# Kernel optimization log

Hardware: AMD Instinct MI355X
Metric: run time of the kernel (lower is better)

The kernel has to match this reference:

```python
import jax, jax.numpy as jnp
import numpy as np
import math

L = 4      # model_layers
D = 512    # model_filters
H = 32     # heads = max(D//16, 1)
DH = D // H  # 16
S = 1024   # dataset_dimension == max_len == seq_len
B = 2
EPS = 1e-5


def setup_inputs() -> dict:
    key = jax.random.key(0)
    ks = jax.random.split(key, 12)
    scale = 0.02
    n = lambda k, shape: jax.random.normal(k, shape, dtype=jnp.float32) * scale
    return {
        "x": jax.random.normal(ks[0], (B, S), dtype=jnp.float32),
        "Winit": n(ks[1], (D,)),               # init_linear weight (1->D)
        "binit": jnp.zeros((D,), jnp.float32),
        "Wq": n(ks[2], (L, D, D)), "bq": jnp.zeros((L, D), jnp.float32),
        "Wk": n(ks[3], (L, D, D)), "bk": jnp.zeros((L, D), jnp.float32),
        "Wv": n(ks[4], (L, D, D)), "bv": jnp.zeros((L, D), jnp.float32),
        "Er": jax.random.normal(ks[5], (L, S, DH), dtype=jnp.float32) * scale,
        "Wlin": n(ks[6], (L, D, D)), "blin": jnp.zeros((L, D), jnp.float32),
        "ln_g": jnp.ones((L, D), jnp.float32), "ln_b": jnp.zeros((L, D), jnp.float32),
        "Wout": n(ks[7], (D, 1)),              # output_linear, no bias
    }


def layernorm(x, g, b):
    mu = jnp.mean(x, axis=-1, keepdims=True)
    var = jnp.mean(jnp.square(x - mu), axis=-1, keepdims=True)
    return (x - mu) * jax.lax.rsqrt(var + EPS) * g + b


def rel_attn(h, Wq, bq, Wk, bk, Wv, bv, Er):
    # h: [B, S, D]
    b_, s_, _ = h.shape
    q = (h @ Wq + bq).reshape(b_, s_, H, DH).transpose(0, 2, 1, 3)  # [B,H,S,dh]
    k = (h @ Wk + bk).reshape(b_, s_, H, DH).transpose(0, 2, 1, 3)
    v = (h @ Wv + bv).reshape(b_, s_, H, DH).transpose(0, 2, 1, 3)
    # relative-position term with skew trick (seq_len == max_len -> full Er)
    QEr = jnp.einsum('bhsd,td->bhst', q, Er)                  # [B,H,S,S]
    padded = jnp.pad(QEr, ((0, 0), (0, 0), (0, 0), (1, 0)))   # pad left of last dim
    Srel = padded.reshape(b_, H, s_ + 1, s_)[:, :, 1:, :]     # skew
    scores = (jnp.einsum('bhsd,bhtd->bhst', q, k) + Srel) / math.sqrt(DH)
    mask = jnp.tril(jnp.ones((s_, s_), dtype=bool))           # causal
    scores = jnp.where(mask, scores, -jnp.inf)
    p = jax.nn.softmax(scores, axis=-1)
    o = jnp.einsum('bhst,bhtd->bhsd', p, v)
    return o.transpose(0, 2, 1, 3).reshape(b_, s_, D)


def reference(x, Winit, binit, Wq, bq, Wk, bk, Wv, bv, Er, Wlin, blin, ln_g, ln_b, Wout):
    # init_linear(1->D) on scalar per position, then exact gelu
    h = jax.nn.gelu(x[..., None] * Winit + binit, approximate=False)  # [B,S,D]
    for l in range(L):
        a = rel_attn(h, Wq[l], bq[l], Wk[l], bk[l], Wv[l], bv[l], Er[l])
        y = layernorm(a @ Wlin[l] + blin[l], ln_g[l], ln_b[l])
        h = h + jax.nn.gelu(y, approximate=False)
    return h.sum(axis=-2) @ Wout  # [B,1]
```

## Files before the change

### kernel.cpp

```cpp
#include <hip/hip_runtime.h>
#include <math.h>

#define NL 4
#define DIM 512
#define NH 32
#define DHD 16
#define SEQ 1024
#define NB 2
#define LN_EPS 1e-5f
#define NEGF (-1e30f)
#define QSC 0.36067376022224085f

typedef _Float16 half4 __attribute__((ext_vector_type(4)));
typedef _Float16 half8 __attribute__((ext_vector_type(8)));
typedef float floatx4 __attribute__((ext_vector_type(4)));

__device__ __forceinline__ float gelu_exact(float x) {
    return 0.5f * x * (1.0f + erff(x * 0.70710678118654752f));
}

__device__ __forceinline__ void async16(const void* g, void* l) {
    __builtin_amdgcn_global_load_lds(
        (const __attribute__((address_space(1))) void*)g,
        (__attribute__((address_space(3))) void*)l, 16, 0, 0);
}

__global__ __launch_bounds__(256) void k_prep_all(const float* __restrict__ Wq,
        const float* __restrict__ Wk, const float* __restrict__ Wv,
        const float* __restrict__ Wlin, const float* __restrict__ bq,
        const float* __restrict__ bk, const float* __restrict__ bv,
        const float* __restrict__ Er, const float* __restrict__ x,
        const float* __restrict__ Wi, const float* __restrict__ bi,
        _Float16* __restrict__ Wqkvt, _Float16* __restrict__ Wlint,
        float* __restrict__ bqkv, _Float16* __restrict__ Erh,
        float* __restrict__ h, _Float16* __restrict__ hf) {
    __shared__ _Float16 lt[64][72];
    const int u = blockIdx.x;
    const int tid = threadIdx.x;
    if (u < 1024) {
        const int kx = u & 7, ny = (u >> 3) & 7, mz = u >> 6;
        const int l = mz >> 2, which = mz & 3;
        const float* src = (which == 0) ? Wq : (which == 1) ? Wk : (which == 2) ? Wv : Wlin;
        src += (size_t)l * 262144;
        const float scale = (which == 0) ? QSC : 1.0f;
        _Float16* dst = (which < 3) ? (Wqkvt + (size_t)l * 786432 + (size_t)which * 262144)
                                    : (Wlint + (size_t)l * 262144);
        const int k0 = kx << 6, n0 = ny << 6;
        #pragma unroll
        for (int p = 0; p < 4; p++) {
            int kl = (p << 4) + (tid >> 4);
            int n4 = (tid & 15) << 2;
            float4 wv = *(const float4*)(src + (size_t)(k0 + kl) * 512 + n0 + n4);
            lt[n4 + 0][kl] = (_Float16)(wv.x * scale);
            lt[n4 + 1][kl] = (_Float16)(wv.y * scale);
            lt[n4 + 2][kl] = (_Float16)(wv.z * scale);
            lt[n4 + 3][kl] = (_Float16)(wv.w * scale);
        }
        __syncthreads();
        int nl = tid >> 2, k16 = (tid & 3) << 4;
        float4* d4 = (float4*)(dst + (size_t)(n0 + nl) * 512 + k0 + k16);
        const float4* s4 = (const float4*)&lt[nl][k16];
        d4[0] = s4[0];
        d4[1] = s4[1];
    } else if (u < 2048) {
        int idx0 = ((u - 1024) << 10) + (tid << 2);
        int d = idx0 & 511, bs = idx0 >> 9;
        float xs = x[bs];
        float4 wv = *(const float4*)(Wi + d);
        float4 bv = *(const float4*)(bi + d);
        float4 r;
        r.x = gelu_exact(xs * wv.x + bv.x);
        r.y = gelu_exact(xs * wv.y + bv.y);
        r.z = gelu_exact(xs * wv.z + bv.z);
        r.w = gelu_exact(xs * wv.w + bv.w);
        *(float4*)(h + idx0) = r;
        half4 rh = {(_Float16)r.x, (_Float16)r.y, (_Float16)r.z, (_Float16)r.w};
        *(half4*)(hf + idx0) = rh;
    } else {
        int idx = ((u - 2048) << 8) + tid;
        if (idx < NL * 1536) {
            int l = idx / 1536, j = idx % 1536;
            int which = j >> 9, jj = j & 511;
            float val = (which == 0) ? bq[l * 512 + jj] * QSC
                      : (which == 1) ? bk[l * 512 + jj] : bv[l * 512 + jj];
            bqkv[idx] = val;
        }
        int e = idx - NL * 1536;
        if (e >= 0 && e < NL * SEQ * DHD) Erh[e] = (_Float16)Er[e];
    }
}

__global__ __launch_bounds__(256) void k_gemm_qkv(const _Float16* __restrict__ A,
        const _Float16* __restrict__ Bt, const float* __restrict__ bias,
        _Float16* __restrict__ o16) {
    __shared__ _Float16 As[64 * 32];
    __shared__ _Float16 Bs[128 * 32];
    const int tid = threadIdx.x;
    const int w = tid >> 6, lane = tid & 63;
    const int nn = lane & 15, qd = lane >> 4;
    const int wm = (w & 1) << 5, wn = (w >> 1) << 6;
    const int m0 = blockIdx.x << 6, n0 = blockIdx.y << 7;
    const int ar = (w << 4) + (lane >> 2);
    const int ac = (lane & 3) << 3;
    const _Float16* Ag  = A  + (size_t)(m0 + ar) * 512 + ac;
    const _Float16* Bg0 = Bt + (size_t)(n0 + (w << 5) + (lane >> 2)) * 512 + ac;
    const _Float16* Bg1 = Bg0 + 16 * 512;
    _Float16* Al  = As + ((w << 4) << 5);
    _Float16* Bl0 = Bs + ((w << 5) << 5);
    _Float16* Bl1 = Bl0 + (16 << 5);
    floatx4 acc[2][4] = {};
    for (int k0 = 0; k0 < 512; k0 += 32) {
        __syncthreads();
        async16(Ag + k0, Al);
        async16(Bg0 + k0, Bl0);
        async16(Bg1 + k0, Bl1);
        __syncthreads();
        half8 af[2], bf[4];
        #pragma unroll
        for (int t = 0; t < 2; t++)
            af[t] = *(const half8*)&As[((wm + (t << 4) + nn) << 5) + (qd << 3)];
        #pragma unroll
        for (int t = 0; t < 4; t++)
            bf[t] = *(const half8*)&Bs[((wn + (t << 4) + nn) << 5) + (qd << 3)];
        #pragma unroll
        for (int ti = 0; ti < 2; ti++)
            #pragma unroll
            for (int tj = 0; tj < 4; tj++)
                acc[ti][tj] = __builtin_amdgcn_mfma_f32_16x16x32_f16(
                        af[ti], bf[tj], acc[ti][tj], 0, 0, 0);
    }
    float bv4[4];
    #pragma unroll
    for (int tj = 0; tj < 4; tj++) bv4[tj] = bias[n0 + wn + (tj << 4) + nn];
    #pragma unroll
    for (int ti = 0; ti < 2; ti++) {
        int rowg = m0 + wm + (ti << 4) + (qd << 2);
        #pragma unroll
        for (int tj = 0; tj < 4; tj++) {
            int colg = n0 + wn + (tj << 4) + nn;
            int which = colg >> 9, ci = colg & 511;
            _Float16* op = o16 + (size_t)which * 1048576 + (size_t)rowg * 512 + ci;
            #pragma unroll
            for (int r = 0; r < 4; r++)
                op[(size_t)r * 512] = (_Float16)(acc[ti][tj][r] + bv4[tj]);
        }
    }
}

__global__ __launch_bounds__(256, 4) void k_attn_mfma(const _Float16* __restrict__ q,
        const _Float16* __restrict__ k, const _Float16* __restrict__ v,
        const _Float16* __restrict__ Er, float* __restrict__ Osp,
        float* __restrict__ ml) {
    __shared__ _Float16 Ks[256][20];
    __shared__ _Float16 Vts[16][264];
    __shared__ float Rel[4][16][84];
    const int tid = threadIdx.x;
    const int wid = tid >> 6, lane = tid & 63;
    const int nn = lane & 15, a4 = (lane >> 4) << 2;
    const int b_ = blockIdx.x >> 5, h_ = blockIdx.x & 31;
    const int qt = blockIdx.y, sp = blockIdx.z;
    const int nch = qt + 1;
    const int hsp = (nch + 1) >> 1;
    const int c_lo = sp ? hsp : 0, c_hi = sp ? nch : hsp;
    const int r0 = qt << 6;
    const int s0w = r0 + (wid << 4);
    const int t_ = tid >> 2, c4 = (tid & 3) << 2;

    half4 qf = *(const half4*)(q + ((size_t)(b_ * SEQ + s0w + nn)) * DIM + h_ * DHD + a4);
    floatx4 O = {0.f, 0.f, 0.f, 0.f};
    float m = NEGF, lsum = 0.f;

    for (int cg = c_lo; cg < c_hi; cg += 4) {
        const int cge = (cg + 4 < c_hi) ? (cg + 4) : c_hi;
        __syncthreads();
        for (int g = 0; g < cge - cg; g++) {
            int rl = (g << 6) + t_;
            size_t gb = ((size_t)(b_ * SEQ + (cg << 6) + rl)) * DIM + h_ * DHD + c4;
            *(half4*)&Ks[rl][c4] = *(const half4*)(k + gb);
            half4 vv4 = *(const half4*)(v + gb);
            Vts[c4 + 0][rl] = vv4.x;
            Vts[c4 + 1][rl] = vv4.y;
            Vts[c4 + 2][rl] = vv4.z;
            Vts[c4 + 3][rl] = vv4.w;
        }
        __syncthreads();
        for (int c = cg; c < cge; c++) {
            const int ct = c << 6;
            const int ctl = (c - cg) << 6;
            const int jbw = 1008 - s0w + ct;
            #pragma unroll
            for (int jt = 0; jt < 5; jt++) {
                int j = jbw + (jt << 4) + nn;
                j = (j < SEQ - 1) ? j : (SEQ - 1);
                half4 ef = *(const half4*)(Er + (size_t)j * DHD + a4);
                floatx4 racc = {0.f, 0.f, 0.f, 0.f};
                racc = __builtin_amdgcn_mfma_f32_16x16x16f16(ef, qf, racc, 0, 0, 0);
                *(floatx4*)&Rel[wid][nn][(jt << 4) + a4] = racc;
            }
            float st[4][4];
            const bool diag = (ct == r0);
            #pragma unroll
            for (int tt = 0; tt < 4; tt++) {
                half4 kf = *(const half4*)&Ks[ctl + (tt << 4) + nn][a4];
                floatx4 sacc = {0.f, 0.f, 0.f, 0.f};
                sacc = __builtin_amdgcn_mfma_f32_16x16x16f16(kf, qf, sacc, 0, 0, 0);
                #pragma unroll
                for (int r = 0; r < 4; r++) {
                    int tl = (tt << 4) + a4 + r;
                    float sv = sacc[r] + Rel[wid][nn][15 - nn + tl];
                    if (diag && (tl > (wid << 4) + nn)) sv = NEGF;
                    st[tt][r] = sv;
                }
            }
            float cmax = NEGF;
            #pragma unroll
            for (int tt = 0; tt < 4; tt++)
                #pragma unroll
                for (int r = 0; r < 4; r++) cmax = fmaxf(cmax, st[tt][r]);
            cmax = fmaxf(cmax, __shfl_xor(cmax, 16));
            cmax = fmaxf(cmax, __shfl_xor(cmax, 32));
            float mnew = fmaxf(m, cmax);
            float alpha = exp2f(m - mnew);
            m = mnew;
            float csum = 0.f;
            half4 pf[4];
            #pragma unroll
            for (int tt = 0; tt < 4; tt++) {
                float p0e = exp2f(st[tt][0] - mnew);
                float p1e = exp2f(st[tt][1] - mnew);
                float p2e = exp2f(st[tt][2] - mnew);
                float p3e = exp2f(st[tt][3] - mnew);
                csum += (p0e + p1e) + (p2e + p3e);
                half4 ph4 = {(_Float16)p0e, (_Float16)p1e, (_Float16)p2e, (_Float16)p3e};
                pf[tt] = ph4;
            }
            csum += __shfl_xor(csum, 16);
            csum += __shfl_xor(csum, 32);
            lsum = lsum * alpha + csum;
            O[0] *= alpha; O[1] *= alpha; O[2] *= alpha; O[3] *= alpha;
            #pragma unroll
            for (int tt = 0; tt < 4; tt++) {
                half4 vf = *(const half4*)&Vts[nn][ctl + (tt << 4) + a4];
                O = __builtin_amdgcn_mfma_f32_16x16x16f16(vf, pf[tt], O, 0, 0, 0);
            }
        }
    }
    float* op = Osp + (size_t)sp * 1048576
              + ((size_t)(b_ * SEQ + s0w + nn)) * DIM + h_ * DHD + a4;
    *(float4*)op = make_float4(O[0], O[1], O[2], O[3]);
    if (a4 == 0) {
        float2* mlp = (float2*)ml;
        mlp[((size_t)((sp * NB + b_) * NH + h_)) * SEQ + s0w + nn] = make_float2(m, lsum);
    }
}

__global__ __launch_bounds__(256) void k_gemm_lin(const float* __restrict__ Osp,
        const float* __restrict__ ml, const _Float16* __restrict__ Bt,
        const float* __restrict__ bias, float* __restrict__ y) {
    __shared__ _Float16 As[64][40];
    __shared__ _Float16 Bs[64 * 32];
    const int tid = threadIdx.x;
    const int w = tid >> 6, lane = tid & 63;
    const int nn = lane & 15, qd = lane >> 4;
    const int wm = (w & 1) << 5, wn = (w >> 1) << 5;
    const int m0 = blockIdx.x << 6, n0 = blockIdx.y << 6;
    const int sr = tid >> 2, sc8 = (tid & 3) << 3;
    const int rowg = m0 + sr;
    const int bb = rowg >> 10, ss = rowg & 1023;
    const float2* mlp = (const float2*)ml;
    const _Float16* Bg = Bt + (size_t)(n0 + (w << 4) + (lane >> 2)) * 512 + ((lane & 3) << 3);
    _Float16* Bl = Bs + ((w << 4) << 5);
    floatx4 acc[2][2] = {};
    for (int k0 = 0; k0 < 512; k0 += 32) {
        __syncthreads();
        async16(Bg + k0, Bl);
        {
            int col = k0 + sc8;
            int hh = col >> 4;
            float2 ml0 = mlp[((size_t)((0 * NB + bb) * NH + hh)) * SEQ + ss];
            float2 ml1 = mlp[((size_t)((1 * NB + bb) * NH + hh)) * SEQ + ss];
            float msx = fmaxf(ml0.x, ml1.x);
            float w0 = exp2f(ml0.x - msx), w1 = exp2f(ml1.x - msx);
            float inv = 1.0f / (ml0.y * w0 + ml1.y * w1);
            w0 *= inv; w1 *= inv;
            const float* p0 = Osp + (size_t)rowg * 512 + col;
            const float* p1 = p0 + 1048576;
            float4 a0 = *(const float4*)(p0);
            float4 a1 = *(const float4*)(p0 + 4);
            float4 b0 = *(const float4*)(p1);
            float4 b1 = *(const float4*)(p1 + 4);
            half8 av = { (_Float16)(a0.x * w0 + b0.x * w1), (_Float16)(a0.y * w0 + b0.y * w1),
                         (_Float16)(a0.z * w0 + b0.z * w1), (_Float16)(a0.w * w0 + b0.w * w1),
                         (_Float16)(a1.x * w0 + b1.x * w1), (_Float16)(a1.y * w0 + b1.y * w1),
                         (_Float16)(a1.z * w0 + b1.z * w1), (_Float16)(a1.w * w0 + b1.w * w1) };
            *(half8*)&As[sr][sc8] = av;
        }
        __syncthreads();
        half8 af[2], bf[2];
        #pragma unroll
        for (int t = 0; t < 2; t++) {
            af[t] = *(const half8*)&As[wm + (t << 4) + nn][qd << 3];
            bf[t] = *(const half8*)&Bs[((wn + (t << 4) + nn) << 5) + (qd << 3)];
        }
        #pragma unroll
        for (int ti = 0; ti < 2; ti++)
            #pragma unroll
            for (int tj = 0; tj < 2; tj++)
                acc[ti][tj] = __builtin_amdgcn_mfma_f32_16x16x32_f16(
                        af[ti], bf[tj], acc[ti][tj], 0, 0, 0);
    }
    float bv2[2];
    #pragma unroll
    for (int tj = 0; tj < 2; tj++) bv2[tj] = bias[n0 + wn + (tj << 4) + nn];
    #pragma unroll
    for (int ti = 0; ti < 2; ti++) {
        int rg = m0 + wm + (ti << 4) + (qd << 2);
        #pragma unroll
        for (int tj = 0; tj < 2; tj++) {
            int colg = n0 + wn + (tj << 4) + nn;
            float* op = y + (size_t)rg * 512 + colg;
            #pragma unroll
            for (int r = 0; r < 4; r++)
                op[(size_t)r * 512] = acc[ti][tj][r] + bv2[tj];
        }
    }
}

__global__ __launch_bounds__(256) void k_ln_gelu_res(const float* __restrict__ y,
        const float* __restrict__ gam, const float* __restrict__ bet,
        float* __restrict__ h, _Float16* __restrict__ hf) {
    __shared__ float red[8];
    int row = blockIdx.x, tid = threadIdx.x;
    const float* yr = y + (size_t)row * DIM;
    float v0 = yr[tid], v1 = yr[tid + 256];
    float sum = v0 + v1, sq = v0 * v0 + v1 * v1;
    #pragma unroll
    for (int off = 32; off > 0; off >>= 1) {
        sum += __shfl_down(sum, off);
        sq  += __shfl_down(sq, off);
    }
    if ((tid & 63) == 0) { red[tid >> 6] = sum; red[4 + (tid >> 6)] = sq; }
    __syncthreads();
    float ts = red[0] + red[1] + red[2] + red[3];
    float tq = red[4] + red[5] + red[6] + red[7];
    float mu = ts * (1.0f / DIM);
    float var = tq * (1.0f / DIM) - mu * mu;
    float rs = rsqrtf(var + LN_EPS);
    float z0 = (v0 - mu) * rs * gam[tid] + bet[tid];
    float z1 = (v1 - mu) * rs * gam[tid + 256] + bet[tid + 256];
    size_t base = (size_t)row * DIM;
    float nh0 = h[base + tid] + gelu_exact(z0);
    float nh1 = h[base + tid + 256] + gelu_exact(z1);
    h[base + tid] = nh0;
    h[base + tid + 256] = nh1;
    hf[base + tid] = (_Float16)nh0;
    hf[base + tid + 256] = (_Float16)nh1;
}

__global__ __launch_bounds__(256) void k_colsum(const float* __restrict__ h,
        float* __restrict__ partial) {
    int bt = blockIdx.x;
    int b_ = bt >> 4, t = bt & 15;
    int tid = threadIdx.x;
    #pragma unroll
    for (int half = 0; half < 2; half++) {
        int d = half * 256 + tid;
        float acc = 0.f;
        for (int i = 0; i < 64; i++)
            acc += h[((size_t)(b_ * SEQ + t * 64 + i)) * DIM + d];
        partial[(size_t)bt * DIM + d] = acc;
    }
}

__global__ __launch_bounds__(256) void k_final(const float* __restrict__ partial,
        const float* __restrict__ Wout, float* __restrict__ out) {
    __shared__ float red[4][2];
    int tid = threadIdx.x;
    float acc0 = 0.f, acc1 = 0.f;
    #pragma unroll
    for (int half = 0; half < 2; half++) {
        int d = half * 256 + tid;
        float w = Wout[d];
        float s0 = 0.f, s1 = 0.f;
        for (int t = 0; t < 16; t++) {
            s0 += partial[t * DIM + d];
            s1 += partial[(16 + t) * DIM + d];
        }
        acc0 += s0 * w;
        acc1 += s1 * w;
    }
    #pragma unroll
    for (int off = 32; off > 0; off >>= 1) {
        acc0 += __shfl_down(acc0, off);
        acc1 += __shfl_down(acc1, off);
    }
    if ((tid & 63) == 0) { red[tid >> 6][0] = acc0; red[tid >> 6][1] = acc1; }
    __syncthreads();
    if (tid == 0) {
        out[0] = red[0][0] + red[1][0] + red[2][0] + red[3][0];
        out[1] = red[0][1] + red[1][1] + red[2][1] + red[3][1];
    }
}

extern "C" void kernel_launch(void* const* d_in, const int* in_sizes, int n_in,
                              void* d_out, int out_size, void* d_ws, size_t ws_size,
                              hipStream_t stream) {
    const float* x    = (const float*)d_in[0];
    const float* Wi   = (const float*)d_in[1];
    const float* bi   = (const float*)d_in[2];
    const float* Wq   = (const float*)d_in[3];
    const float* bq   = (const float*)d_in[4];
    const float* Wk   = (const float*)d_in[5];
    const float* bk   = (const float*)d_in[6];
    const float* Wv   = (const float*)d_in[7];
    const float* bv   = (const float*)d_in[8];
    const float* Er   = (const float*)d_in[9];
    const float* Wlin = (const float*)d_in[10];
    const float* blin = (const float*)d_in[11];
    const float* lng  = (const float*)d_in[12];
    const float* lnb  = (const float*)d_in[13];
    const float* Wout = (const float*)d_in[14];
    float* out = (float*)d_out;

    float* ws = (float*)d_ws;
    const size_t N1 = 1048576;
    float*     h     = ws;
    _Float16*  hf    = (_Float16*)(ws + N1);
    _Float16*  qh    = (_Float16*)(ws + N1 + N1/2);
    float*     y     = ws + 3 * N1;
    _Float16*  Wqkvt = (_Float16*)(ws + 4 * N1 + N1/2);
    _Float16*  Wlint = (_Float16*)(ws + 6 * N1);
    float*     bqkv  = ws + 6 * N1 + N1/2;
    _Float16*  Erh   = (_Float16*)(ws + 6 * N1 + N1/2 + 8192);
    float*     Osp   = ws + 7 * N1;
    float*     ml    = ws + 9 * N1;
    float*     pa    = ws + 9 * N1 + 262144 + 64;

    k_prep_all<<<dim3(2328), dim3(256), 0, stream>>>(Wq, Wk, Wv, Wlin, bq, bk, bv,
            Er, x, Wi, bi, Wqkvt, Wlint, bqkv, Erh, h, hf);
    for (int l = 0; l < NL; l++) {
        k_gemm_qkv<<<dim3(32, 12), dim3(256), 0, stream>>>(
                hf, Wqkvt + (size_t)l * 786432, bqkv + l * 1536, qh);
        k_attn_mfma<<<dim3(NB * NH, 16, 2), dim3(256), 0, stream>>>(
                qh, qh + 1048576, qh + 2097152, Erh + (size_t)l * 16384, Osp, ml);
        k_gemm_lin<<<dim3(32, 8), dim3(256), 0, stream>>>(
                Osp, ml, Wlint + (size_t)l * 262144, blin + l * 512, y);
        k_ln_gelu_res<<<dim3(NB * SEQ), dim3(256), 0, stream>>>(
                y, lng + l * 512, lnb + l * 512, h, hf);
    }
    k_colsum<<<dim3(32), dim3(256), 0, stream>>>(h, pa);
    k_final<<<dim3(1), dim3(256), 0, stream>>>(pa, Wout, out);
}
```

Baseline: 336.8 us.

## Pair causal query tiles in attention, emit fp16 output, widen GEMM k-steps, warp-per-row LN

Attention no longer splits the key range into two halves merged later. Each block now processes a balanced pair of query tiles (y and 15-y) and writes normalized fp16 output directly, so the fp32 partial outputs and max/sum buffers go away. The linear GEMM therefore becomes a plain fp16 async-load GEMM. The QKV and linear GEMMs load 64-wide k-slices per barrier pair, halving synchronizations. LayerNorm uses one wavefront per row with vectorized float4 loads and no shared-memory reduction. The cost is half as many attention blocks, which means less parallelism, plus larger shared-memory tiles in the GEMMs.

```diff
diff --git a/kernel.cpp b/kernel.cpp
--- a/kernel.cpp
+++ b/kernel.cpp
@@ -93,41 +93,44 @@
 __global__ __launch_bounds__(256) void k_gemm_qkv(const _Float16* __restrict__ A,
         const _Float16* __restrict__ Bt, const float* __restrict__ bias,
         _Float16* __restrict__ o16) {
-    __shared__ _Float16 As[64 * 32];
-    __shared__ _Float16 Bs[128 * 32];
+    __shared__ _Float16 As[2 * 64 * 32];
+    __shared__ _Float16 Bs[2 * 128 * 32];
     const int tid = threadIdx.x;
     const int w = tid >> 6, lane = tid & 63;
     const int nn = lane & 15, qd = lane >> 4;
     const int wm = (w & 1) << 5, wn = (w >> 1) << 6;
     const int m0 = blockIdx.x << 6, n0 = blockIdx.y << 7;
-    const int ar = (w << 4) + (lane >> 2);
-    const int ac = (lane & 3) << 3;
-    const _Float16* Ag  = A  + (size_t)(m0 + ar) * 512 + ac;
-    const _Float16* Bg0 = Bt + (size_t)(n0 + (w << 5) + (lane >> 2)) * 512 + ac;
-    const _Float16* Bg1 = Bg0 + 16 * 512;
-    _Float16* Al  = As + ((w << 4) << 5);
-    _Float16* Bl0 = Bs + ((w << 5) << 5);
-    _Float16* Bl1 = Bl0 + (16 << 5);
+    const int l2r = lane >> 2, l2c = (lane & 3) << 3;
+    const _Float16* Ag = A + (size_t)(m0 + (w << 4) + l2r) * 512 + l2c;
+    const _Float16* Bg = Bt + (size_t)(n0 + (w << 5) + l2r) * 512 + l2c;
+    _Float16* Al = As + (w << 9);
+    _Float16* Bl = Bs + (w << 10);
     floatx4 acc[2][4] = {};
-    for (int k0 = 0; k0 < 512; k0 += 32) {
-        __syncthreads();
-        async16(Ag + k0, Al);
-        async16(Bg0 + k0, Bl0);
-        async16(Bg1 + k0, Bl1);
-        __syncthreads();
-        half8 af[2], bf[4];
-        #pragma unroll
-        for (int t = 0; t < 2; t++)
-            af[t] = *(const half8*)&As[((wm + (t << 4) + nn) << 5) + (qd << 3)];
-        #pragma unroll
-        for (int t = 0; t < 4; t++)
-            bf[t] = *(const half8*)&Bs[((wn + (t << 4) + nn) << 5) + (qd << 3)];
-        #pragma unroll
-        for (int ti = 0; ti < 2; ti++)
-            #pragma unroll
-            for (int tj = 0; tj < 4; tj++)
-                acc[ti][tj] = __builtin_amdgcn_mfma_f32_16x16x32_f16(
-                        af[ti], bf[tj], acc[ti][tj], 0, 0, 0);
+    for (int k0 = 0; k0 < 512; k0 += 64) {
+        __syncthreads();
+        #pragma unroll
+        for (int p = 0; p < 2; p++) {
+            async16(Ag + k0 + (p << 5), Al + (p << 11));
+            async16(Bg + k0 + (p << 5), Bl + (p << 12));
+            async16(Bg + k0 + (p << 5) + (16 << 9), Bl + (p << 12) + (16 << 5));
+        }
+        __syncthreads();
+        #pragma unroll
+        for (int ks = 0; ks < 2; ks++) {
+            half8 af[2], bf[4];
+            #pragma unroll
+            for (int t = 0; t < 2; t++)
+                af[t] = *(const half8*)&As[(ks << 11) + ((wm + (t << 4) + nn) << 5) + (qd << 3)];
+            #pragma unroll
+            for (int t = 0; t < 4; t++)
+                bf[t] = *(const half8*)&Bs[(ks << 12) + ((wn + (t << 4) + nn) << 5) + (qd << 3)];
+            #pragma unroll
+            for (int ti = 0; ti < 2; ti++)
+                #pragma unroll
+                for (int tj = 0; tj < 4; tj++)
+                    acc[ti][tj] = __builtin_amdgcn_mfma_f32_16x16x32_f16(
+                            af[ti], bf[tj], acc[ti][tj], 0, 0, 0);
+        }
     }
     float bv4[4];
     #pragma unroll
@@ -147,35 +150,99 @@
     }
 }
 
+__global__ __launch_bounds__(256) void k_gemm_lin(const _Float16* __restrict__ A,
+        const _Float16* __restrict__ Bt, const float* __restrict__ bias,
+        float* __restrict__ y) {
+    __shared__ _Float16 As[2 * 64 * 32];
+    __shared__ _Float16 Bs[2 * 64 * 32];
+    const int tid = threadIdx.x;
+    const int w = tid >> 6, lane = tid & 63;
+    const int nn = lane & 15, qd = lane >> 4;
+    const int wm = (w & 1) << 5, wn = (w >> 1) << 5;
+    const int m0 = blockIdx.x << 6, n0 = blockIdx.y << 6;
+    const int l2r = lane >> 2, l2c = (lane & 3) << 3;
+    const _Float16* Ag = A + (size_t)(m0 + (w << 4) + l2r) * 512 + l2c;
+    const _Float16* Bg = Bt + (size_t)(n0 + (w << 4) + l2r) * 512 + l2c;
+    _Float16* Al = As + (w << 9);
+    _Float16* Bl = Bs + (w << 9);
+    floatx4 acc[2][2] = {};
+    for (int k0 = 0; k0 < 512; k0 += 64) {
+        __syncthreads();
+        #pragma unroll
+        for (int p = 0; p < 2; p++) {
+            async16(Ag + k0 + (p << 5), Al + (p << 11));
+            async16(Bg + k0 + (p << 5), Bl + (p << 11));
+        }
+        __syncthreads();
+        #pragma unroll
+        for (int ks = 0; ks < 2; ks++) {
+            half8 af[2], bf[2];
+            #pragma unroll
+            for (int t = 0; t < 2; t++) {
+                af[t] = *(const half8*)&As[(ks << 11) + ((wm + (t << 4) + nn) << 5) + (qd << 3)];
+                bf[t] = *(const half8*)&Bs[(ks << 11) + ((wn + (t << 4) + nn) << 5) + (qd << 3)];
+            }
+            #pragma unroll
+            for (int ti = 0; ti < 2; ti++)
+                #pragma unroll
+                for (int tj = 0; tj < 2; tj++)
+                    acc[ti][tj] = __builtin_amdgcn_mfma_f32_16x16x32_f16(
+                            af[ti], bf[tj], acc[ti][tj], 0, 0, 0);
+        }
+    }
+    float bv2[2];
+    #pragma unroll
+    for (int tj = 0; tj < 2; tj++) bv2[tj] = bias[n0 + wn + (tj << 4) + nn];
+    #pragma unroll
+    for (int ti = 0; ti < 2; ti++) {
+        int rg = m0 + wm + (ti << 4) + (qd << 2);
+        #pragma unroll
+        for (int tj = 0; tj < 2; tj++) {
+            int colg = n0 + wn + (tj << 4) + nn;
+            float* op = y + (size_t)rg * 512 + colg;
+            #pragma unroll
+            for (int r = 0; r < 4; r++)
+                op[(size_t)r * 512] = acc[ti][tj][r] + bv2[tj];
+        }
+    }
+}
+
 __global__ __launch_bounds__(256, 4) void k_attn_mfma(const _Float16* __restrict__ q,
         const _Float16* __restrict__ k, const _Float16* __restrict__ v,
-        const _Float16* __restrict__ Er, float* __restrict__ Osp,
-        float* __restrict__ ml) {
+        const _Float16* __restrict__ Er, _Float16* __restrict__ aout) {
     __shared__ _Float16 Ks[256][20];
-    __shared__ _Float16 Vts[16][264];
-    __shared__ float Rel[4][16][84];
+    __shared__ _Float16 Vts[16][268];
+    __shared__ float Rel[4][16][80];
     const int tid = threadIdx.x;
     const int wid = tid >> 6, lane = tid & 63;
     const int nn = lane & 15, a4 = (lane >> 4) << 2;
     const int b_ = blockIdx.x >> 5, h_ = blockIdx.x & 31;
-    const int qt = blockIdx.y, sp = blockIdx.z;
-    const int nch = qt + 1;
-    const int hsp = (nch + 1) >> 1;
-    const int c_lo = sp ? hsp : 0, c_hi = sp ? nch : hsp;
-    const int r0 = qt << 6;
-    const int s0w = r0 + (wid << 4);
+    const int y = blockIdx.y;
     const int t_ = tid >> 2, c4 = (tid & 3) << 2;
-
-    half4 qf = *(const half4*)(q + ((size_t)(b_ * SEQ + s0w + nn)) * DIM + h_ * DHD + a4);
-    floatx4 O = {0.f, 0.f, 0.f, 0.f};
-    float m = NEGF, lsum = 0.f;
-
-    for (int cg = c_lo; cg < c_hi; cg += 4) {
-        const int cge = (cg + 4 < c_hi) ? (cg + 4) : c_hi;
-        __syncthreads();
-        for (int g = 0; g < cge - cg; g++) {
+    const int r0p[2] = {64 * y, 64 * (15 - y)};
+    const int R = r0p[1] + 64;
+
+    half4 qf[2];
+    floatx4 O[2];
+    float m[2], lsum[2];
+    #pragma unroll
+    for (int ph = 0; ph < 2; ph++) {
+        int s0w = r0p[ph] + (wid << 4);
+        qf[ph] = *(const half4*)(q + ((size_t)(b_ * SEQ + s0w + nn)) * DIM + h_ * DHD + a4);
+        O[ph] = (floatx4){0.f, 0.f, 0.f, 0.f};
+        m[ph] = NEGF;
+        lsum[ph] = 0.f;
+    }
+
+    for (int part = 0; part < 4; part++) {
+        const int p0 = part << 8;
+        if (p0 >= R) break;
+        const int pend = (R < p0 + 256) ? R : (p0 + 256);
+        __syncthreads();
+        const int ng = (pend - p0) >> 6;
+        for (int g = 0; g < ng; g++) {
             int rl = (g << 6) + t_;
-            size_t gb = ((size_t)(b_ * SEQ + (cg << 6) + rl)) * DIM + h_ * DHD + c4;
+            size_t gb = ((size_t)(b_ * SEQ + p0 + rl)) * DIM + h_ * DHD + c4;
             *(half4*)&Ks[rl][c4] = *(const half4*)(k + gb);
             half4 vv4 = *(const half4*)(v + gb);
             Vts[c4 + 0][rl] = vv4.x;
@@ -184,177 +251,123 @@
             Vts[c4 + 3][rl] = vv4.w;
         }
         __syncthreads();
-        for (int c = cg; c < cge; c++) {
-            const int ct = c << 6;
-            const int ctl = (c - cg) << 6;
-            const int jbw = 1008 - s0w + ct;
-            #pragma unroll
-            for (int jt = 0; jt < 5; jt++) {
-                int j = jbw + (jt << 4) + nn;
-                j = (j < SEQ - 1) ? j : (SEQ - 1);
-                half4 ef = *(const half4*)(Er + (size_t)j * DHD + a4);
-                floatx4 racc = {0.f, 0.f, 0.f, 0.f};
-                racc = __builtin_amdgcn_mfma_f32_16x16x16f16(ef, qf, racc, 0, 0, 0);
-                *(floatx4*)&Rel[wid][nn][(jt << 4) + a4] = racc;
-            }
-            float st[4][4];
-            const bool diag = (ct == r0);
-            #pragma unroll
-            for (int tt = 0; tt < 4; tt++) {
-                half4 kf = *(const half4*)&Ks[ctl + (tt << 4) + nn][a4];
-                floatx4 sacc = {0.f, 0.f, 0.f, 0.f};
-                sacc = __builtin_amdgcn_mfma_f32_16x16x16f16(kf, qf, sacc, 0, 0, 0);
-                #pragma unroll
-                for (int r = 0; r < 4; r++) {
-                    int tl = (tt << 4) + a4 + r;
-                    float sv = sacc[r] + Rel[wid][nn][15 - nn + tl];
-                    if (diag && (tl > (wid << 4) + nn)) sv = NEGF;
-                    st[tt][r] = sv;
+        #pragma unroll
+        for (int ph = 0; ph < 2; ph++) {
+            const int r0 = r0p[ph];
+            const int s0w = r0 + (wid << 4);
+            const int hi = (r0 + 64 < pend) ? (r0 + 64) : pend;
+            for (int ct = p0; ct < hi; ct += 64) {
+                const int ctl = ct - p0;
+                const int jbw = 1008 - s0w + ct;
+                #pragma unroll
+                for (int jt = 0; jt < 5; jt++) {
+                    int j = jbw + (jt << 4) + nn;
+                    j = (j < SEQ - 1) ? j : (SEQ - 1);
+                    half4 ef = *(const half4*)(Er + (size_t)j * DHD + a4);
+                    floatx4 racc = {0.f, 0.f, 0.f, 0.f};
+                    racc = __builtin_amdgcn_mfma_f32_16x16x16f16(ef, qf[ph], racc, 0, 0, 0);
+                    *(floatx4*)&Rel[wid][nn][(jt << 4) + a4] = racc;
+                }
+                float st[4][4];
+                const bool diag = (ct == r0);
+                #pragma unroll
+                for (int tt = 0; tt < 4; tt++) {
+                    half4 kf = *(const half4*)&Ks[ctl + (tt << 4) + nn][a4];
+                    floatx4 sacc = {0.f, 0.f, 0.f, 0.f};
+                    sacc = __builtin_amdgcn_mfma_f32_16x16x16f16(kf, qf[ph], sacc, 0, 0, 0);
+                    #pragma unroll
+                    for (int r = 0; r < 4; r++) {
+                        int tl = (tt << 4) + a4 + r;
+                        float sv = sacc[r] + Rel[wid][nn][15 - nn + tl];
+                        if (diag && (tl > (wid << 4) + nn)) sv = NEGF;
+                        st[tt][r] = sv;
+                    }
+                }
+                float cmax = NEGF;
+                #pragma unroll
+                for (int tt = 0; tt < 4; tt++)
+                    #pragma unroll
+                    for (int r = 0; r < 4; r++) cmax = fmaxf(cmax, st[tt][r]);
+                cmax = fmaxf(cmax, __shfl_xor(cmax, 16));
+                cmax = fmaxf(cmax, __shfl_xor(cmax, 32));
+                float mnew = fmaxf(m[ph], cmax);
+                float alpha = exp2f(m[ph] - mnew);
+                m[ph] = mnew;
+                float csum = 0.f;
+                half4 pf[4];
+                #pragma unroll
+                for (int tt = 0; tt < 4; tt++) {
+                    float p0e = exp2f(st[tt][0] - mnew);
+                    float p1e = exp2f(st[tt][1] - mnew);
+                    float p2e = exp2f(st[tt][2] - mnew);
+                    float p3e = exp2f(st[tt][3] - mnew);
+                    csum += (p0e + p1e) + (p2e + p3e);
+                    half4 ph4 = {(_Float16)p0e, (_Float16)p1e, (_Float16)p2e, (_Float16)p3e};
+                    pf[tt] = ph4;
+                }
+                lsum[ph] = lsum[ph] * alpha + csum;
+                O[ph][0] *= alpha; O[ph][1] *= alpha; O[ph][2] *= alpha; O[ph][3] *= alpha;
+                #pragma unroll
+                for (int tt = 0; tt < 4; tt++) {
+                    half4 vf = *(const half4*)&Vts[nn][ctl + (tt << 4) + a4];
+                    O[ph] = __builtin_amdgcn_mfma_f32_16x16x16f16(vf, pf[tt], O[ph], 0, 0, 0);
                 }
             }
-            float cmax = NEGF;
-            #pragma unroll
-            for (int tt = 0; tt < 4; tt++)
-                #pragma unroll
-                for (int r = 0; r < 4; r++) cmax = fmaxf(cmax, st[tt][r]);
-            cmax = fmaxf(cmax, __shfl_xor(cmax, 16));
-            cmax = fmaxf(cmax, __shfl_xor(cmax, 32));
-            float mnew = fmaxf(m, cmax);
-            float alpha = exp2f(m - mnew);
-            m = mnew;
-            float csum = 0.f;
-            half4 pf[4];
-            #pragma unroll
-            for (int tt = 0; tt < 4; tt++) {
-                float p0e = exp2f(st[tt][0] - mnew);
-                float p1e = exp2f(st[tt][1] - mnew);
-                float p2e = exp2f(st[tt][2] - mnew);
-                float p3e = exp2f(st[tt][3] - mnew);
-                csum += (p0e + p1e) + (p2e + p3e);
-                half4 ph4 = {(_Float16)p0e, (_Float16)p1e, (_Float16)p2e, (_Float16)p3e};
-                pf[tt] = ph4;
-            }
-            csum += __shfl_xor(csum, 16);
-            csum += __shfl_xor(csum, 32);
-            lsum = lsum * alpha + csum;
-            O[0] *= alpha; O[1] *= alpha; O[2] *= alpha; O[3] *= alpha;
-            #pragma unroll
-            for (int tt = 0; tt < 4; tt++) {
-                half4 vf = *(const half4*)&Vts[nn][ctl + (tt << 4) + a4];
-                O = __builtin_amdgcn_mfma_f32_16x16x16f16(vf, pf[tt], O, 0, 0, 0);
-            }
-        }
-    }
-    float* op = Osp + (size_t)sp * 1048576
-              + ((size_t)(b_ * SEQ + s0w + nn)) * DIM + h_ * DHD + a4;
-    *(float4*)op = make_float4(O[0], O[1], O[2], O[3]);
-    if (a4 == 0) {
-        float2* mlp = (float2*)ml;
-        mlp[((size_t)((sp * NB + b_) * NH + h_)) * SEQ + s0w + nn] = make_float2(m, lsum);
-    }
-}
-
-__global__ __launch_bounds__(256) void k_gemm_lin(const float* __restrict__ Osp,
-        const float* __restrict__ ml, const _Float16* __restrict__ Bt,
-        const float* __restrict__ bias, float* __restrict__ y) {
-    __shared__ _Float16 As[64][40];
-    __shared__ _Float16 Bs[64 * 32];
-    const int tid = threadIdx.x;
-    const int w = tid >> 6, lane = tid & 63;
-    const int nn = lane & 15, qd = lane >> 4;
-    const int wm = (w & 1) << 5, wn = (w >> 1) << 5;
-    const int m0 = blockIdx.x << 6, n0 = blockIdx.y << 6;
-    const int sr = tid >> 2, sc8 = (tid & 3) << 3;
-    const int rowg = m0 + sr;
-    const int bb = rowg >> 10, ss = rowg & 1023;
-    const float2* mlp = (const float2*)ml;
-    const _Float16* Bg = Bt + (size_t)(n0 + (w << 4) + (lane >> 2)) * 512 + ((lane & 3) << 3);
-    _Float16* Bl = Bs + ((w << 4) << 5);
-    floatx4 acc[2][2] = {};
-    for (int k0 = 0; k0 < 512; k0 += 32) {
-        __syncthreads();
-        async16(Bg + k0, Bl);
-        {
-            int col = k0 + sc8;
-            int hh = col >> 4;
-            float2 ml0 = mlp[((size_t)((0 * NB + bb) * NH + hh)) * SEQ + ss];
-            float2 ml1 = mlp[((size_t)((1 * NB + bb) * NH + hh)) * SEQ + ss];
-            float msx = fmaxf(ml0.x, ml1.x);
-            float w0 = exp2f(ml0.x - msx), w1 = exp2f(ml1.x - msx);
-            float inv = 1.0f / (ml0.y * w0 + ml1.y * w1);
-            w0 *= inv; w1 *= inv;
-            const float* p0 = Osp + (size_t)rowg * 512 + col;
-            const float* p1 = p0 + 1048576;
-            float4 a0 = *(const float4*)(p0);
-            float4 a1 = *(const float4*)(p0 + 4);
-            float4 b0 = *(const float4*)(p1);
-            float4 b1 = *(const float4*)(p1 + 4);
-            half8 av = { (_Float16)(a0.x * w0 + b0.x * w1), (_Float16)(a0.y * w0 + b0.y * w1),
-                         (_Float16)(a0.z * w0 + b0.z * w1), (_Float16)(a0.w * w0 + b0.w * w1),
-                         (_Float16)(a1.x * w0 + b1.x * w1), (_Float16)(a1.y * w0 + b1.y * w1),
-                         (_Float16)(a1.z * w0 + b1.z * w1), (_Float16)(a1.w * w0 + b1.w * w1) };
-            *(half8*)&As[sr][sc8] = av;
-        }
-        __syncthreads();
-        half8 af[2], bf[2];
-        #pragma unroll
-        for (int t = 0; t < 2; t++) {
-            af[t] = *(const half8*)&As[wm + (t << 4) + nn][qd << 3];
-            bf[t] = *(const half8*)&Bs[((wn + (t << 4) + nn) << 5) + (qd << 3)];
-        }
-        #pragma unroll
-        for (int ti = 0; ti < 2; ti++)
-            #pragma unroll
-            for (int tj = 0; tj < 2; tj++)
-                acc[ti][tj] = __builtin_amdgcn_mfma_f32_16x16x32_f16(
-                        af[ti], bf[tj], acc[ti][tj], 0, 0, 0);
-    }
-    float bv2[2];
-    #pragma unroll
-    for (int tj = 0; tj < 2; tj++) bv2[tj] = bias[n0 + wn + (tj << 4) + nn];
-    #pragma unroll
-    for (int ti = 0; ti < 2; ti++) {
-        int rg = m0 + wm + (ti << 4) + (qd << 2);
-        #pragma unroll
-        for (int tj = 0; tj < 2; tj++) {
-            int colg = n0 + wn + (tj << 4) + nn;
-            float* op = y + (size_t)rg * 512 + colg;
-            #pragma unroll
-            for (int r = 0; r < 4; r++)
-                op[(size_t)r * 512] = acc[ti][tj][r] + bv2[tj];
-        }
+        }
+    }
+    #pragma unroll
+    for (int ph = 0; ph < 2; ph++) {
+        float lt = lsum[ph];
+        lt += __shfl_xor(lt, 16);
+        lt += __shfl_xor(lt, 32);
+        float linv = 1.0f / lt;
+        int s0w = r0p[ph] + (wid << 4);
+        half4 ov = { (_Float16)(O[ph][0] * linv), (_Float16)(O[ph][1] * linv),
+                     (_Float16)(O[ph][2] * linv), (_Float16)(O[ph][3] * linv) };
+        *(half4*)(aout + ((size_t)(b_ * SEQ + s0w + nn)) * DIM + h_ * DHD + a4) = ov;
     }
 }
 
 __global__ __launch_bounds__(256) void k_ln_gelu_res(const float* __restrict__ y,
         const float* __restrict__ gam, const float* __restrict__ bet,
         float* __restrict__ h, _Float16* __restrict__ hf) {
-    __shared__ float red[8];
-    int row = blockIdx.x, tid = threadIdx.x;
-    const float* yr = y + (size_t)row * DIM;
-    float v0 = yr[tid], v1 = yr[tid + 256];
-    float sum = v0 + v1, sq = v0 * v0 + v1 * v1;
+    int row = (blockIdx.x << 2) + (threadIdx.x >> 6);
+    int lane = threadIdx.x & 63;
+    const float* yr = y + (size_t)row * DIM + (lane << 3);
+    float4 v0 = *(const float4*)(yr);
+    float4 v1 = *(const float4*)(yr + 4);
+    float sum = (v0.x + v0.y) + (v0.z + v0.w) + (v1.x + v1.y) + (v1.z + v1.w);
+    float sq = v0.x*v0.x + v0.y*v0.y + v0.z*v0.z + v0.w*v0.w
+             + v1.x*v1.x + v1.y*v1.y + v1.z*v1.z + v1.w*v1.w;
     #pragma unroll
     for (int off = 32; off > 0; off >>= 1) {
-        sum += __shfl_down(sum, off);
-        sq  += __shfl_down(sq, off);
-    }
-    if ((tid & 63) == 0) { red[tid >> 6] = sum; red[4 + (tid >> 6)] = sq; }
-    __syncthreads();
-    float ts = red[0] + red[1] + red[2] + red[3];
-    float tq = red[4] + red[5] + red[6] + red[7];
-    float mu = ts * (1.0f / DIM);
-    float var = tq * (1.0f / DIM) - mu * mu;
+        sum += __shfl_xor(sum, off);
+        sq  += __shfl_xor(sq, off);
+    }
+    float mu = sum * (1.0f / DIM);
+    float var = sq * (1.0f / DIM) - mu * mu;
     float rs = rsqrtf(var + LN_EPS);
-    float z0 = (v0 - mu) * rs * gam[tid] + bet[tid];
-    float z1 = (v1 - mu) * rs * gam[tid + 256] + bet[tid + 256];
-    size_t base = (size_t)row * DIM;
-    float nh0 = h[base + tid] + gelu_exact(z0);
-    float nh1 = h[base + tid + 256] + gelu_exact(z1);
-    h[base + tid] = nh0;
-    h[base + tid + 256] = nh1;
-    hf[base + tid] = (_Float16)nh0;
-    hf[base + tid + 256] = (_Float16)nh1;
+    float4 g0 = *(const float4*)(gam + (lane << 3));
+    float4 g1 = *(const float4*)(gam + (lane << 3) + 4);
+    float4 b0 = *(const float4*)(bet + (lane << 3));
+    float4 b1 = *(const float4*)(bet + (lane << 3) + 4);
+    float* hr = h + (size_t)row * DIM + (lane << 3);
+    float4 h0 = *(const float4*)(hr);
+    float4 h1 = *(const float4*)(hr + 4);
+    float o[8];
+    o[0] = h0.x + gelu_exact((v0.x - mu) * rs * g0.x + b0.x);
+    o[1] = h0.y + gelu_exact((v0.y - mu) * rs * g0.y + b0.y);
+    o[2] = h0.z + gelu_exact((v0.z - mu) * rs * g0.z + b0.z);
+    o[3] = h0.w + gelu_exact((v0.w - mu) * rs * g0.w + b0.w);
+    o[4] = h1.x + gelu_exact((v1.x - mu) * rs * g1.x + b1.x);
+    o[5] = h1.y + gelu_exact((v1.y - mu) * rs * g1.y + b1.y);
+    o[6] = h1.z + gelu_exact((v1.z - mu) * rs * g1.z + b1.z);
+    o[7] = h1.w + gelu_exact((v1.w - mu) * rs * g1.w + b1.w);
+    *(float4*)(hr)     = make_float4(o[0], o[1], o[2], o[3]);
+    *(float4*)(hr + 4) = make_float4(o[4], o[5], o[6], o[7]);
+    half8 oh = {(_Float16)o[0], (_Float16)o[1], (_Float16)o[2], (_Float16)o[3],
+                (_Float16)o[4], (_Float16)o[5], (_Float16)o[6], (_Float16)o[7]};
+    *(half8*)(hf + (size_t)row * DIM + (lane << 3)) = oh;
 }
 
 __global__ __launch_bounds__(256) void k_colsum(const float* __restrict__ h,
@@ -427,25 +440,24 @@
     float*     h     = ws;
     _Float16*  hf    = (_Float16*)(ws + N1);
     _Float16*  qh    = (_Float16*)(ws + N1 + N1/2);
-    float*     y     = ws + 3 * N1;
+    _Float16*  ah    = (_Float16*)(ws + 3 * N1);
+    float*     y     = ws + 3 * N1 + N1/2;
     _Float16*  Wqkvt = (_Float16*)(ws + 4 * N1 + N1/2);
     _Float16*  Wlint = (_Float16*)(ws + 6 * N1);
     float*     bqkv  = ws + 6 * N1 + N1/2;
     _Float16*  Erh   = (_Float16*)(ws + 6 * N1 + N1/2 + 8192);
-    float*     Osp   = ws + 7 * N1;
-    float*     ml    = ws + 9 * N1;
-    float*     pa    = ws + 9 * N1 + 262144 + 64;
+    float*     pa    = ws + 6 * N1 + N1/2 + 8192 + 32768;
 
     k_prep_all<<<dim3(2328), dim3(256), 0, stream>>>(Wq, Wk, Wv, Wlin, bq, bk, bv,
             Er, x, Wi, bi, Wqkvt, Wlint, bqkv, Erh, h, hf);
     for (int l = 0; l < NL; l++) {
         k_gemm_qkv<<<dim3(32, 12), dim3(256), 0, stream>>>(
                 hf, Wqkvt + (size_t)l * 786432, bqkv + l * 1536, qh);
-        k_attn_mfma<<<dim3(NB * NH, 16, 2), dim3(256), 0, stream>>>(
-                qh, qh + 1048576, qh + 2097152, Erh + (size_t)l * 16384, Osp, ml);
+        k_attn_mfma<<<dim3(NB * NH, 8), dim3(256), 0, stream>>>(
+                qh, qh + 1048576, qh + 2097152, Erh + (size_t)l * 16384, ah);
         k_gemm_lin<<<dim3(32, 8), dim3(256), 0, stream>>>(
-                Osp, ml, Wlint + (size_t)l * 262144, blin + l * 512, y);
-        k_ln_gelu_res<<<dim3(NB * SEQ), dim3(256), 0, stream>>>(
+                ah, Wlint + (size_t)l * 262144, blin + l * 512, y);
+        k_ln_gelu_res<<<dim3(512), dim3(256), 0, stream>>>(
                 y, lng + l * 512, lnb + l * 512, h, hf);
     }
     k_colsum<<<dim3(32), dim3(256), 0, stream>>>(h, pa);
```

Result: faster. 315.0 us (-6.5%).
